# Optimization experiments

Hardware: AMD Instinct MI355X
Metric: run time of the kernel (lower is better)

Reference implementation:

```python
import jax, jax.numpy as jnp
import numpy as np

NUM_EXPERTS = 8
TOP_K = 2
D_IN = 1024
D_OUT = 1024
N_TOKENS = 8192


def setup_inputs() -> dict:
    key = jax.random.key(0)
    ks = jax.random.split(key, 7)
    s_in = 1.0 / np.sqrt(D_IN)
    s_out = 1.0 / np.sqrt(D_OUT)
    return {
        "x": jax.random.normal(ks[0], (N_TOKENS, D_IN), dtype=jnp.float32),
        # stacked expert params: fc1 [E, D_in, D_out], fc2 [E, D_out, D_out]
        "W1": jax.random.uniform(ks[1], (NUM_EXPERTS, D_IN, D_OUT), jnp.float32, -s_in, s_in),
        "b1": jax.random.uniform(ks[2], (NUM_EXPERTS, D_OUT), jnp.float32, -s_in, s_in),
        "W2": jax.random.uniform(ks[3], (NUM_EXPERTS, D_OUT, D_OUT), jnp.float32, -s_out, s_out),
        "b2": jax.random.uniform(ks[4], (NUM_EXPERTS, D_OUT), jnp.float32, -s_out, s_out),
        "Wg": jax.random.uniform(ks[5], (D_IN, NUM_EXPERTS), jnp.float32, -s_in, s_in),
        "bg": jax.random.uniform(ks[6], (NUM_EXPERTS,), jnp.float32, -s_in, s_in),
    }


def reference(x, W1, b1, W2, b2, Wg, bg):
    n = x.shape[0]
    # gating
    gate_logits = x @ Wg + bg                      # [N, E]
    gate_weights = jax.nn.softmax(gate_logits, axis=1)
    if TOP_K < NUM_EXPERTS:
        topk_vals, topk_idx = jax.lax.top_k(gate_weights, TOP_K)  # [N, K]
        rows = jnp.arange(n)[:, None]
        gate_weights = jnp.zeros_like(gate_weights).at[rows, topk_idx].set(topk_vals)
    # dense all-expert MLP fan-out (faithful to the original wasteful compute)
    h = jax.nn.relu(jnp.einsum('nd,edh->enh', x, W1) + b1[:, None, :])  # [E, N, H]
    y = jnp.einsum('enh,eho->eno', h, W2) + b2[:, None, :]               # [E, N, O]
    # weighted combine over experts
    out = jnp.einsum('ne,eno->no', gate_weights, y)                      # [N, O]
    return out
```

## Files before the change

### kernel.cpp

```cpp
#include <hip/hip_runtime.h>

#define NUM_E 8
#define N_TOK 8192
#define DIM 1024

typedef __attribute__((ext_vector_type(8))) short short8;
typedef __attribute__((ext_vector_type(4))) float f32x4;

__device__ __forceinline__ unsigned short f2bf(float f) {
  unsigned int u = __float_as_uint(f);
  u = (u + 0x7fffu + ((u >> 16) & 1u)) >> 16;
  return (unsigned short)u;
}

__device__ __forceinline__ void async16(const unsigned short* g, unsigned short* l) {
  __builtin_amdgcn_global_load_lds((const __attribute__((address_space(1))) void*)g,
                                   (__attribute__((address_space(3))) void*)l,
                                   16, 0, 0);
}

__global__ __launch_bounds__(256) void prep_kernel(
    const float* __restrict__ W1, const float* __restrict__ W2,
    unsigned short* __restrict__ W1T, unsigned short* __restrict__ W2T,
    const float* __restrict__ x, const float* __restrict__ Wg,
    const float* __restrict__ bg, int* __restrict__ tok_top,
    float2* __restrict__ tok_wts, unsigned short* __restrict__ xb) {
  __shared__ float s[64][65];
  if (blockIdx.x < 4096) {
    const int bx  = blockIdx.x;
    const int mat = bx >> 8;
    const int tk  = (bx >> 4) & 15;
    const int tn  = bx & 15;
    const float* src;
    unsigned short* dst;
    if (mat < 8) { src = W1 + (size_t)mat * (DIM * DIM); dst = W1T + (size_t)mat * (DIM * DIM); }
    else         { src = W2 + (size_t)(mat - 8) * (DIM * DIM); dst = W2T + (size_t)(mat - 8) * (DIM * DIM); }
    const int k0 = tk * 64, n0 = tn * 64;
    const int t = threadIdx.x;
    {
      const int rr = t >> 4;
      const int c4 = (t & 15) * 4;
#pragma unroll
      for (int i = 0; i < 4; ++i) {
        const int k = i * 16 + rr;
        float4 v = *(const float4*)&src[(size_t)(k0 + k) * DIM + n0 + c4];
        s[c4 + 0][k] = v.x; s[c4 + 1][k] = v.y;
        s[c4 + 2][k] = v.z; s[c4 + 3][k] = v.w;
      }
    }
    __syncthreads();
    {
      const int kq = (t & 7) * 8;
      const int nn = t >> 3;
#pragma unroll
      for (int r = 0; r < 2; ++r) {
        const int n = r * 32 + nn;
        union { unsigned short us[8]; uint4 v; } o;
#pragma unroll
        for (int j = 0; j < 8; ++j) o.us[j] = f2bf(s[n][kq + j]);
        *(uint4*)(dst + (size_t)(n0 + n) * DIM + k0 + kq) = o.v;
      }
    }
  } else {
    const int wave = threadIdx.x >> 6;
    const int lane = threadIdx.x & 63;
    const int n = (blockIdx.x - 4096) * 4 + wave;
    const float4* xr = (const float4*)(x + (size_t)n * DIM);
    unsigned short* xbr = xb + (size_t)n * DIM;
    float acc[NUM_E];
#pragma unroll
    for (int e = 0; e < NUM_E; ++e) acc[e] = 0.f;
#pragma unroll
    for (int it = 0; it < 4; ++it) {
      float4 xv = xr[it * 64 + lane];
      const float4* wr = (const float4*)Wg + (size_t)(it * 256 + lane * 4) * 2;
      float xs[4] = {xv.x, xv.y, xv.z, xv.w};
      union { unsigned short u[4]; uint2 v; } oo;
      oo.u[0] = f2bf(xv.x); oo.u[1] = f2bf(xv.y);
      oo.u[2] = f2bf(xv.z); oo.u[3] = f2bf(xv.w);
      *(uint2*)(xbr + it * 256 + lane * 4) = oo.v;
#pragma unroll
      for (int dd = 0; dd < 4; ++dd) {
        float4 wa = wr[dd * 2 + 0];
        float4 wb = wr[dd * 2 + 1];
        acc[0] += xs[dd] * wa.x; acc[1] += xs[dd] * wa.y;
        acc[2] += xs[dd] * wa.z; acc[3] += xs[dd] * wa.w;
        acc[4] += xs[dd] * wb.x; acc[5] += xs[dd] * wb.y;
        acc[6] += xs[dd] * wb.z; acc[7] += xs[dd] * wb.w;
      }
    }
#pragma unroll
    for (int e = 0; e < NUM_E; ++e)
#pragma unroll
      for (int off = 32; off > 0; off >>= 1)
        acc[e] += __shfl_down(acc[e], off);
    if (lane == 0) {
      float p[NUM_E];
      float mx = -1e30f;
#pragma unroll
      for (int e = 0; e < NUM_E; ++e) { p[e] = acc[e] + bg[e]; mx = fmaxf(mx, p[e]); }
      float ss = 0.f;
#pragma unroll
      for (int e = 0; e < NUM_E; ++e) { p[e] = expf(p[e] - mx); ss += p[e]; }
      float inv = 1.f / ss;
      int i0 = 0;
#pragma unroll
      for (int e = 1; e < NUM_E; ++e) if (p[e] > p[i0]) i0 = e;
      int i1 = (i0 == 0) ? 1 : 0;
#pragma unroll
      for (int e = 0; e < NUM_E; ++e) if (e != i0 && p[e] > p[i1]) i1 = e;
      tok_top[n] = i0 | (i1 << 8);
      tok_wts[n] = make_float2(p[i0] * inv, p[i1] * inv);
    }
  }
}

__global__ __launch_bounds__(1024) void gate2_kernel(const int* __restrict__ tok_top,
                                                     const float2* __restrict__ tok_wts,
                                                     int* __restrict__ counts,
                                                     int* __restrict__ tok_idx,
                                                     float* __restrict__ tok_w) {
  const int e = blockIdx.x;
  const int t = threadIdx.x;
  const int lane = t & 63;
  const int wave = t >> 6;
  __shared__ int wsum[16];
  __shared__ int blocktot;
  int match[8];
  float w[8];
  int cnt = 0;
#pragma unroll
  for (int j = 0; j < 8; ++j) {
    int n = t * 8 + j;
    int top = tok_top[n];
    float2 ww = tok_wts[n];
    bool m0 = (top & 0xff) == e;
    bool m1 = ((top >> 8) & 0xff) == e;
    match[j] = (m0 || m1) ? 1 : 0;
    w[j] = m0 ? ww.x : ww.y;
    cnt += match[j];
  }
  int inc = cnt;
#pragma unroll
  for (int off = 1; off < 64; off <<= 1) {
    int v = __shfl_up(inc, off);
    if (lane >= off) inc += v;
  }
  if (lane == 63) wsum[wave] = inc;
  __syncthreads();
  if (t < 16) {
    int v = wsum[t];
    int s = v;
#pragma unroll
    for (int off = 1; off < 16; off <<= 1) {
      int u = __shfl_up(s, off);
      if (lane >= off) s += u;
    }
    wsum[t] = s - v;
    if (t == 15) blocktot = s;
  }
  __syncthreads();
  int slot = wsum[wave] + inc - cnt;
#pragma unroll
  for (int j = 0; j < 8; ++j) {
    if (match[j]) {
      tok_idx[e * N_TOK + slot] = t * 8 + j;
      tok_w[e * N_TOK + slot] = w[j];
      slot++;
    }
  }
  if (t == 0) counts[e] = blocktot;
}


template <bool FC1>
__global__ __launch_bounds__(256, 4) void moe_gemm_kernel(
    const unsigned short* __restrict__ A_src,
    const unsigned short* __restrict__ wT,
    const float* __restrict__ bias,
    const int* __restrict__ counts,
    const int* __restrict__ tok_idx,
    const float* __restrict__ tok_w,
    unsigned short* __restrict__ h_out,
    float* __restrict__ out)
{
  const int bid = blockIdx.x;
  const int xcd = bid & 7;
  const int mt  = xcd * 17 + (bid >> 6);
  const int nt  = (bid >> 3) & 7;

  int e = -1, m0 = 0, base = 0;
  {
    int acc_tiles = 0, acc_rows = 0;
#pragma unroll
    for (int i = 0; i < NUM_E; ++i) {
      int c = counts[i];
      int t = (c + 127) >> 7;
      if (mt >= acc_tiles && mt < acc_tiles + t) {
        e = i; m0 = (mt - acc_tiles) * 128; base = acc_rows;
      }
      acc_tiles += t;
      acc_rows += t * 128;
    }
  }
  if (e < 0) return;
  const int count = counts[e];
  const int n0 = nt * 128;

  const int tid  = threadIdx.x;
  const int wave = tid >> 6;
  const int lane = tid & 63;
  const int l15  = lane & 15;
  const int quad = lane >> 4;
  const int wm   = wave & 1;
  const int wn   = wave >> 1;

  __shared__ unsigned short sA[2 * 4096];
  __shared__ unsigned short sB[2 * 4096];
  __shared__ int   s_tok[128];
  __shared__ float s_w[128];

  if (!FC1 && tid < 128) {
    int slot = m0 + tid;
    int cs = slot < count ? slot : count - 1;
    s_tok[tid] = tok_idx[e * N_TOK + cs];
    s_w[tid]   = slot < count ? tok_w[e * N_TOK + slot] : 0.f;
  }

  const int r0 = 32 * wave + l15;
  const int r1 = r0 + 16;
  size_t aOff0, aOff1;
  if (FC1) {
    int s0 = m0 + r0; s0 = s0 < count ? s0 : count - 1;
    int s1 = m0 + r1; s1 = s1 < count ? s1 : count - 1;
    aOff0 = (size_t)tok_idx[e * N_TOK + s0] * DIM;
    aOff1 = (size_t)tok_idx[e * N_TOK + s1] * DIM;
  } else {
    aOff0 = (size_t)(base + m0 + r0) * DIM;
    aOff1 = (size_t)(base + m0 + r1) * DIM;
  }
  const unsigned short* wte = wT + (size_t)e * DIM * DIM;
  const size_t bOff0 = (size_t)(n0 + r0) * DIM;
  const size_t bOff1 = (size_t)(n0 + r1) * DIM;
  const int kl = quad * 8;
  const int c0 = (2 * wave + 0) * 512;
  const int c1 = (2 * wave + 1) * 512;

  const f32x4 vzero = {0.f, 0.f, 0.f, 0.f};
  f32x4 acc[4][4];
#pragma unroll
  for (int i = 0; i < 4; ++i)
#pragma unroll
    for (int j = 0; j < 4; ++j) acc[i][j] = vzero;

  for (int k0 = 0; k0 < DIM; k0 += 64) {
    async16(A_src + aOff0 + k0 + kl,      &sA[c0]);
    async16(A_src + aOff1 + k0 + kl,      &sA[c1]);
    async16(A_src + aOff0 + k0 + 32 + kl, &sA[4096 + c0]);
    async16(A_src + aOff1 + k0 + 32 + kl, &sA[4096 + c1]);
    async16(wte + bOff0 + k0 + kl,        &sB[c0]);
    async16(wte + bOff1 + k0 + kl,        &sB[c1]);
    async16(wte + bOff0 + k0 + 32 + kl,   &sB[4096 + c0]);
    async16(wte + bOff1 + k0 + 32 + kl,   &sB[4096 + c1]);
    __syncthreads();
#pragma unroll
    for (int s = 0; s < 2; ++s) {
      short8 af[4], bfr[4];
#pragma unroll
      for (int i = 0; i < 4; ++i)
        af[i] = *(const short8*)&sA[s * 4096 + (wm * 4 + i) * 512 + lane * 8];
#pragma unroll
      for (int j = 0; j < 4; ++j)
        bfr[j] = *(const short8*)&sB[s * 4096 + (wn * 4 + j) * 512 + lane * 8];
#pragma unroll
      for (int i = 0; i < 4; ++i)
#pragma unroll
        for (int j = 0; j < 4; ++j)
          acc[i][j] = __builtin_amdgcn_mfma_f32_16x16x32_bf16(af[i], bfr[j], acc[i][j], 0, 0, 0);
    }
    __syncthreads();
  }

  float bv[4];
#pragma unroll
  for (int j = 0; j < 4; ++j)
    bv[j] = bias[e * DIM + n0 + (wn * 4 + j) * 16 + l15];

  if (FC1) {
#pragma unroll
    for (int i = 0; i < 4; ++i) {
      const int rbase = (wm * 4 + i) * 16 + quad * 4;
#pragma unroll
      for (int r = 0; r < 4; ++r) {
        const int slot = m0 + rbase + r;
        if (slot < count) {
          unsigned short* hp = h_out + (size_t)(base + slot) * DIM + n0;
#pragma unroll
          for (int j = 0; j < 4; ++j) {
            float v = acc[i][j][r] + bv[j];
            v = v > 0.f ? v : 0.f;
            hp[(wn * 4 + j) * 16 + l15] = f2bf(v);
          }
        }
      }
    }
  } else {
#pragma unroll
    for (int i = 0; i < 4; ++i) {
      const int rbase = (wm * 4 + i) * 16 + quad * 4;
#pragma unroll
      for (int r = 0; r < 4; ++r) {
        const int slot = m0 + rbase + r;
        if (slot < count) {
          const int rl = rbase + r;
          const int tok = s_tok[rl];
          const float w = s_w[rl];
          float* op = out + (size_t)tok * DIM + n0;
#pragma unroll
          for (int j = 0; j < 4; ++j) {
            float v = acc[i][j][r] + bv[j];
            atomicAdd(&op[(wn * 4 + j) * 16 + l15], w * v);
          }
        }
      }
    }
  }
}


extern "C" void kernel_launch(void* const* d_in, const int* in_sizes, int n_in,
                              void* d_out, int out_size, void* d_ws, size_t ws_size,
                              hipStream_t stream) {
  const float* x  = (const float*)d_in[0];
  const float* W1 = (const float*)d_in[1];
  const float* b1 = (const float*)d_in[2];
  const float* W2 = (const float*)d_in[3];
  const float* b2 = (const float*)d_in[4];
  const float* Wg = (const float*)d_in[5];
  const float* bg = (const float*)d_in[6];
  float* out = (float*)d_out;

  char* ws = (char*)d_ws;
  int*            counts  = (int*)(ws);
  int*            tok_idx = (int*)(ws + 1024);
  float*          tok_w   = (float*)(ws + 263168);
  unsigned short* xb      = (unsigned short*)(ws + 525312);
  unsigned short* w1t     = (unsigned short*)(ws + 525312 + 16777216ull);
  unsigned short* w2t     = (unsigned short*)(ws + 525312 + 2ull * 16777216ull);
  unsigned short* hb      = (unsigned short*)(ws + 525312 + 3ull * 16777216ull);
  size_t gate_off = 525312 + 3ull * 16777216ull + 35651584ull;
  int*            tok_top = (int*)(ws + gate_off);
  float2*         tok_wts = (float2*)(ws + gate_off + 32768);

  hipMemsetAsync(d_out, 0, (size_t)N_TOK * DIM * sizeof(float), stream);

  prep_kernel<<<4096 + 2048, 256, 0, stream>>>(W1, W2, w1t, w2t,
                                               x, Wg, bg, tok_top, tok_wts, xb);
  gate2_kernel<<<NUM_E, 1024, 0, stream>>>(tok_top, tok_wts, counts, tok_idx, tok_w);
  moe_gemm_kernel<true><<<1088, 256, 0, stream>>>(
      xb, w1t, b1, counts, tok_idx, tok_w, hb, nullptr);
  moe_gemm_kernel<false><<<1088, 256, 0, stream>>>(
      hb, w2t, b2, counts, tok_idx, tok_w, nullptr, out);
}
```

Before: 368.4 us.

## Fold output zeroing into gating kernel and merge token bucketing into weight prep

Removes the separate memset of the output and instead zeroes it inside a new gating/x-conversion kernel. The expert bucketing (scan over routed tokens) now runs as 8 extra blocks of the weight transpose kernel, so the former single-wave-of-8-blocks gate2 launch disappears and overlaps with the weight conversion. The bucketing uses 256 threads with 32 tokens each and a bitmask, re-reading token data on the write pass. This cuts one launch and one memset, at the cost of a less parallel scan per expert.

```diff
diff --git a/kernel.cpp b/kernel.cpp
--- a/kernel.cpp
+++ b/kernel.cpp
@@ -19,13 +19,78 @@
                                    16, 0, 0);
 }
 
-__global__ __launch_bounds__(256) void prep_kernel(
+__global__ __launch_bounds__(256) void prep_gate_kernel(
+    const float* __restrict__ x, const float* __restrict__ Wg,
+    const float* __restrict__ bg, int* __restrict__ tok_top,
+    float2* __restrict__ tok_wts, unsigned short* __restrict__ xb,
+    float* __restrict__ out) {
+  {
+    float4* oz = (float4*)(out + (size_t)blockIdx.x * 4096);
+    const float4 z4 = {0.f, 0.f, 0.f, 0.f};
+#pragma unroll
+    for (int i = 0; i < 4; ++i) oz[i * 256 + threadIdx.x] = z4;
+  }
+  const int wave = threadIdx.x >> 6;
+  const int lane = threadIdx.x & 63;
+  const int n = blockIdx.x * 4 + wave;
+  const float4* xr = (const float4*)(x + (size_t)n * DIM);
+  unsigned short* xbr = xb + (size_t)n * DIM;
+  float acc[NUM_E];
+#pragma unroll
+  for (int e = 0; e < NUM_E; ++e) acc[e] = 0.f;
+#pragma unroll
+  for (int it = 0; it < 4; ++it) {
+    float4 xv = xr[it * 64 + lane];
+    const float4* wr = (const float4*)Wg + (size_t)(it * 256 + lane * 4) * 2;
+    float xs[4] = {xv.x, xv.y, xv.z, xv.w};
+    union { unsigned short u[4]; uint2 v; } oo;
+    oo.u[0] = f2bf(xv.x); oo.u[1] = f2bf(xv.y);
+    oo.u[2] = f2bf(xv.z); oo.u[3] = f2bf(xv.w);
+    *(uint2*)(xbr + it * 256 + lane * 4) = oo.v;
+#pragma unroll
+    for (int dd = 0; dd < 4; ++dd) {
+      float4 wa = wr[dd * 2 + 0];
+      float4 wb = wr[dd * 2 + 1];
+      acc[0] += xs[dd] * wa.x; acc[1] += xs[dd] * wa.y;
+      acc[2] += xs[dd] * wa.z; acc[3] += xs[dd] * wa.w;
+      acc[4] += xs[dd] * wb.x; acc[5] += xs[dd] * wb.y;
+      acc[6] += xs[dd] * wb.z; acc[7] += xs[dd] * wb.w;
+    }
+  }
+#pragma unroll
+  for (int e = 0; e < NUM_E; ++e)
+#pragma unroll
+    for (int off = 32; off > 0; off >>= 1)
+      acc[e] += __shfl_down(acc[e], off);
+  if (lane == 0) {
+    float p[NUM_E];
+    float mx = -1e30f;
+#pragma unroll
+    for (int e = 0; e < NUM_E; ++e) { p[e] = acc[e] + bg[e]; mx = fmaxf(mx, p[e]); }
+    float ss = 0.f;
+#pragma unroll
+    for (int e = 0; e < NUM_E; ++e) { p[e] = expf(p[e] - mx); ss += p[e]; }
+    float inv = 1.f / ss;
+    int i0 = 0;
+#pragma unroll
+    for (int e = 1; e < NUM_E; ++e) if (p[e] > p[i0]) i0 = e;
+    int i1 = (i0 == 0) ? 1 : 0;
+#pragma unroll
+    for (int e = 0; e < NUM_E; ++e) if (e != i0 && p[e] > p[i1]) i1 = e;
+    tok_top[n] = i0 | (i1 << 8);
+    tok_wts[n] = make_float2(p[i0] * inv, p[i1] * inv);
+  }
+}
+
+__global__ __launch_bounds__(256) void prep_w_gate2_kernel(
     const float* __restrict__ W1, const float* __restrict__ W2,
     unsigned short* __restrict__ W1T, unsigned short* __restrict__ W2T,
-    const float* __restrict__ x, const float* __restrict__ Wg,
-    const float* __restrict__ bg, int* __restrict__ tok_top,
-    float2* __restrict__ tok_wts, unsigned short* __restrict__ xb) {
+    const int* __restrict__ tok_top, const float2* __restrict__ tok_wts,
+    int* __restrict__ counts, int* __restrict__ tok_idx,
+    float* __restrict__ tok_w) {
   __shared__ float s[64][65];
+  __shared__ int wsum[4];
+  __shared__ int btot;
   if (blockIdx.x < 4096) {
     const int bx  = blockIdx.x;
     const int mat = bx >> 8;
@@ -62,114 +127,54 @@
       }
     }
   } else {
-    const int wave = threadIdx.x >> 6;
-    const int lane = threadIdx.x & 63;
-    const int n = (blockIdx.x - 4096) * 4 + wave;
-    const float4* xr = (const float4*)(x + (size_t)n * DIM);
-    unsigned short* xbr = xb + (size_t)n * DIM;
-    float acc[NUM_E];
-#pragma unroll
-    for (int e = 0; e < NUM_E; ++e) acc[e] = 0.f;
-#pragma unroll
-    for (int it = 0; it < 4; ++it) {
-      float4 xv = xr[it * 64 + lane];
-      const float4* wr = (const float4*)Wg + (size_t)(it * 256 + lane * 4) * 2;
-      float xs[4] = {xv.x, xv.y, xv.z, xv.w};
-      union { unsigned short u[4]; uint2 v; } oo;
-      oo.u[0] = f2bf(xv.x); oo.u[1] = f2bf(xv.y);
-      oo.u[2] = f2bf(xv.z); oo.u[3] = f2bf(xv.w);
-      *(uint2*)(xbr + it * 256 + lane * 4) = oo.v;
-#pragma unroll
-      for (int dd = 0; dd < 4; ++dd) {
-        float4 wa = wr[dd * 2 + 0];
-        float4 wb = wr[dd * 2 + 1];
-        acc[0] += xs[dd] * wa.x; acc[1] += xs[dd] * wa.y;
-        acc[2] += xs[dd] * wa.z; acc[3] += xs[dd] * wa.w;
-        acc[4] += xs[dd] * wb.x; acc[5] += xs[dd] * wb.y;
-        acc[6] += xs[dd] * wb.z; acc[7] += xs[dd] * wb.w;
-      }
-    }
-#pragma unroll
-    for (int e = 0; e < NUM_E; ++e)
-#pragma unroll
-      for (int off = 32; off > 0; off >>= 1)
-        acc[e] += __shfl_down(acc[e], off);
-    if (lane == 0) {
-      float p[NUM_E];
-      float mx = -1e30f;
-#pragma unroll
-      for (int e = 0; e < NUM_E; ++e) { p[e] = acc[e] + bg[e]; mx = fmaxf(mx, p[e]); }
-      float ss = 0.f;
-#pragma unroll
-      for (int e = 0; e < NUM_E; ++e) { p[e] = expf(p[e] - mx); ss += p[e]; }
-      float inv = 1.f / ss;
-      int i0 = 0;
-#pragma unroll
-      for (int e = 1; e < NUM_E; ++e) if (p[e] > p[i0]) i0 = e;
-      int i1 = (i0 == 0) ? 1 : 0;
-#pragma unroll
-      for (int e = 0; e < NUM_E; ++e) if (e != i0 && p[e] > p[i1]) i1 = e;
-      tok_top[n] = i0 | (i1 << 8);
-      tok_wts[n] = make_float2(p[i0] * inv, p[i1] * inv);
-    }
-  }
-}
-
-__global__ __launch_bounds__(1024) void gate2_kernel(const int* __restrict__ tok_top,
-                                                     const float2* __restrict__ tok_wts,
-                                                     int* __restrict__ counts,
-                                                     int* __restrict__ tok_idx,
-                                                     float* __restrict__ tok_w) {
-  const int e = blockIdx.x;
-  const int t = threadIdx.x;
-  const int lane = t & 63;
-  const int wave = t >> 6;
-  __shared__ int wsum[16];
-  __shared__ int blocktot;
-  int match[8];
-  float w[8];
-  int cnt = 0;
-#pragma unroll
-  for (int j = 0; j < 8; ++j) {
-    int n = t * 8 + j;
-    int top = tok_top[n];
-    float2 ww = tok_wts[n];
-    bool m0 = (top & 0xff) == e;
-    bool m1 = ((top >> 8) & 0xff) == e;
-    match[j] = (m0 || m1) ? 1 : 0;
-    w[j] = m0 ? ww.x : ww.y;
-    cnt += match[j];
-  }
-  int inc = cnt;
-#pragma unroll
-  for (int off = 1; off < 64; off <<= 1) {
-    int v = __shfl_up(inc, off);
-    if (lane >= off) inc += v;
-  }
-  if (lane == 63) wsum[wave] = inc;
-  __syncthreads();
-  if (t < 16) {
-    int v = wsum[t];
-    int s = v;
-#pragma unroll
-    for (int off = 1; off < 16; off <<= 1) {
-      int u = __shfl_up(s, off);
-      if (lane >= off) s += u;
-    }
-    wsum[t] = s - v;
-    if (t == 15) blocktot = s;
-  }
-  __syncthreads();
-  int slot = wsum[wave] + inc - cnt;
-#pragma unroll
-  for (int j = 0; j < 8; ++j) {
-    if (match[j]) {
-      tok_idx[e * N_TOK + slot] = t * 8 + j;
-      tok_w[e * N_TOK + slot] = w[j];
-      slot++;
-    }
-  }
-  if (t == 0) counts[e] = blocktot;
+    const int e = blockIdx.x - 4096;
+    const int t = threadIdx.x;
+    const int lane = t & 63;
+    const int wave = t >> 6;
+    unsigned mask = 0;
+    int cnt = 0;
+#pragma unroll 8
+    for (int j = 0; j < 32; ++j) {
+      int top = tok_top[t * 32 + j];
+      bool m = ((top & 0xff) == e) || (((top >> 8) & 0xff) == e);
+      mask |= (unsigned)m << j;
+      cnt += m;
+    }
+    int inc = cnt;
+#pragma unroll
+    for (int off = 1; off < 64; off <<= 1) {
+      int v = __shfl_up(inc, off);
+      if (lane >= off) inc += v;
+    }
+    if (lane == 63) wsum[wave] = inc;
+    __syncthreads();
+    if (t < 4) {
+      int v = wsum[t];
+      int ssum = v;
+#pragma unroll
+      for (int off = 1; off < 4; off <<= 1) {
+        int u = __shfl_up(ssum, off);
+        if (lane >= off) ssum += u;
+      }
+      wsum[t] = ssum - v;
+      if (t == 3) btot = ssum;
+    }
+    __syncthreads();
+    int slot = wsum[wave] + inc - cnt;
+#pragma unroll 8
+    for (int j = 0; j < 32; ++j) {
+      if ((mask >> j) & 1u) {
+        int n = t * 32 + j;
+        int top = tok_top[n];
+        float2 ww = tok_wts[n];
+        bool m0 = (top & 0xff) == e;
+        tok_idx[e * N_TOK + slot] = n;
+        tok_w[e * N_TOK + slot] = m0 ? ww.x : ww.y;
+        slot++;
+      }
+    }
+    if (t == 0) counts[e] = btot;
+  }
 }
 
 
@@ -352,11 +357,9 @@
   int*            tok_top = (int*)(ws + gate_off);
   float2*         tok_wts = (float2*)(ws + gate_off + 32768);
 
-  hipMemsetAsync(d_out, 0, (size_t)N_TOK * DIM * sizeof(float), stream);
-
-  prep_kernel<<<4096 + 2048, 256, 0, stream>>>(W1, W2, w1t, w2t,
-                                               x, Wg, bg, tok_top, tok_wts, xb);
-  gate2_kernel<<<NUM_E, 1024, 0, stream>>>(tok_top, tok_wts, counts, tok_idx, tok_w);
+  prep_gate_kernel<<<2048, 256, 0, stream>>>(x, Wg, bg, tok_top, tok_wts, xb, out);
+  prep_w_gate2_kernel<<<4104, 256, 0, stream>>>(W1, W2, w1t, w2t,
+                                                tok_top, tok_wts, counts, tok_idx, tok_w);
   moe_gemm_kernel<true><<<1088, 256, 0, stream>>>(
       xb, w1t, b1, counts, tok_idx, tok_w, hb, nullptr);
   moe_gemm_kernel<false><<<1088, 256, 0, stream>>>(
```

New measurement: 378.9 us. 2.9% more time.
